# Performance work log

Hardware: AMD Instinct MI355X
Metric: run time of the kernel (lower is better)

## Reference

```python
import jax, jax.numpy as jnp
import numpy as np

D_MODEL = 768
MIMO_RANK = 4


def setup_inputs() -> dict:
    key = jax.random.key(0)
    ks = jax.random.split(key, 6)
    B, T, D, R = 2, 2048, D_MODEL, MIMO_RANK
    x = jax.random.normal(ks[0], (B, T, D), dtype=jnp.float32)
    norm_w = jnp.ones((D,), dtype=jnp.float32)
    W_in = jax.random.normal(ks[1], (D * R * 2, D), dtype=jnp.float32) * 0.02
    W_out = jax.random.normal(ks[2], (D, D), dtype=jnp.float32) * 0.02
    a_param = jax.random.normal(ks[3], (D, R, 2), dtype=jnp.float32) * 0.12
    b_param = jax.random.normal(ks[4], (D, R, 2), dtype=jnp.float32) * 0.15
    c_param = jax.random.normal(ks[5], (D, R, 2), dtype=jnp.float32) * 0.15
    return {"x": x, "norm_w": norm_w, "W_in": W_in, "W_out": W_out,
            "a_param": a_param, "b_param": b_param, "c_param": c_param}


def reference(x, norm_w, W_in, W_out, a_param, b_param, c_param):
    B, T, D = x.shape
    R = a_param.shape[1]
    # RMSNorm
    xn = x * jax.lax.rsqrt(jnp.mean(x * x, axis=-1, keepdims=True) + 1e-6) * norm_w
    # in_proj -> interleaved complex MIMO input u: [B,T,D,R,2]
    u = (xn @ W_in.T).reshape(B, T, D, R, 2)
    # coefficients (tanh-bounded; |a| scaled by 0.97 for stability)
    a = jnp.tanh(a_param) * 0.97
    b = jnp.tanh(b_param)
    c = jnp.tanh(c_param)
    ac = jax.lax.complex(a[..., 0], a[..., 1])  # [D,R]
    bc = jax.lax.complex(b[..., 0], b[..., 1])
    cc = jax.lax.complex(c[..., 0], c[..., 1])
    uc = jax.lax.complex(u[..., 0], u[..., 1])  # [B,T,D,R]
    # linear complex recurrence s_t = a * s_{t-1} + b * u_t, zero init state,
    # parallelized with an associative scan over time.
    bu = bc[None, None] * uc
    A = jnp.broadcast_to(ac[None, None], bu.shape)

    def comb(l, r):
        return (l[0] * r[0], r[0] * l[1] + r[1])

    _, s = jax.lax.associative_scan(comb, (A, bu), axis=1)  # [B,T,D,R] complex
    # output mix: real part of c * h, summed over MIMO rank -> [B,T,D]
    y = jnp.real(cc[None, None] * s).sum(axis=-1)
    return y @ W_out.T
```

## Files before the change

kernel.cpp:

```cpp
#include <hip/hip_runtime.h>
#include <hip/hip_bf16.h>
#include <stdint.h>

#define BATCH 2
#define TT 2048
#define DM 768
#define RR 4
#define M_TOK 4096
#define NFEAT 6144
#define NCH 6144
#define CHUNK 64
#define NCHUNK 32

typedef __attribute__((ext_vector_type(8))) short short8;
typedef __attribute__((ext_vector_type(4))) float float4v;

__device__ inline float bf2f(uint32_t bits16) {
    union { uint32_t u; float f; } x; x.u = bits16 << 16; return x.f;
}

typedef const __attribute__((address_space(1))) void* gptr_t;
typedef __attribute__((address_space(3))) void* lptr_t;

__device__ inline void async_ld16(const void* g, void* l) {
    __builtin_amdgcn_global_load_lds((gptr_t)(uintptr_t)g, (lptr_t)(uintptr_t)l,
                                     16, 0, 0);
}

__device__ inline void store_c(__hip_bfloat16* C, size_t idx, float v) {
    C[idx] = __float2bfloat16(v);
}
__device__ inline void store_c(float* C, size_t idx, float v) { C[idx] = v; }

__device__ inline uint2 pack4bf(float a, float b, float c, float d) {
    union { __hip_bfloat16 h[4]; uint2 u; } o;
    o.h[0] = __float2bfloat16(a); o.h[1] = __float2bfloat16(b);
    o.h[2] = __float2bfloat16(c); o.h[3] = __float2bfloat16(d);
    return o.u;
}

__device__ inline float2 cmul(float2 a, float2 b) {
    return make_float2(a.x * b.x - a.y * b.y, a.x * b.y + a.y * b.x);
}
__device__ inline float2 cmad(float2 a, float2 b, float2 c) {
    return make_float2(a.x * b.x - a.y * b.y + c.x,
                       a.x * b.y + a.y * b.x + c.y);
}
__device__ inline float2 csq(float2 a) {
    return make_float2(a.x * a.x - a.y * a.y, 2.f * a.x * a.y);
}

__device__ inline void cstep(float& sr, float& si, float2 a, float2 bb,
                             uint32_t uw) {
    float ur = bf2f(uw & 0xffffu), ui = bf2f(uw >> 16);
    float tr = bb.x * ur - bb.y * ui;
    float ti = bb.x * ui + bb.y * ur;
    float nr = a.x * sr - a.y * si + tr;
    float ni = a.x * si + a.y * sr + ti;
    sr = nr; si = ni;
}

__global__ __launch_bounds__(256) void prep_rms(
    const float* __restrict__ x, const float* __restrict__ w,
    const float* __restrict__ W_in, const float* __restrict__ W_out,
    const float* __restrict__ ap, const float* __restrict__ bp,
    const float* __restrict__ cp,
    __hip_bfloat16* __restrict__ xn,
    __hip_bfloat16* __restrict__ Win_bf, __hip_bfloat16* __restrict__ Wout_bf,
    float2* __restrict__ ac, float2* __restrict__ bc,
    float2* __restrict__ cc, float2* __restrict__ aL) {
    int bid = blockIdx.x;
    int tid = threadIdx.x;
    if (bid < M_TOK) {
        __shared__ float wsum[3];
        float4 v = make_float4(0.f, 0.f, 0.f, 0.f);
        if (tid < 192) v = ((const float4*)(x + (size_t)bid * DM))[tid];
        float ss = v.x * v.x + v.y * v.y + v.z * v.z + v.w * v.w;
        #pragma unroll
        for (int o = 1; o < 64; o <<= 1) ss += __shfl_xor(ss, o);
        if (tid < 192 && (tid & 63) == 0) wsum[tid >> 6] = ss;
        __syncthreads();
        if (tid < 192) {
            float tot = wsum[0] + wsum[1] + wsum[2];
            float scale = rsqrtf(tot * (1.f / DM) + 1e-6f);
            float4 wv = ((const float4*)w)[tid];
            ((uint2*)(xn + (size_t)bid * DM))[tid] =
                pack4bf(v.x * scale * wv.x, v.y * scale * wv.y,
                        v.z * scale * wv.z, v.w * scale * wv.w);
        }
        return;
    }
    const int N1 = NFEAT * DM / 4;
    const int N2 = DM * DM / 4;
    int i = (bid - M_TOK) * 256 + tid;
    if (i < N1) {
        float4 v = ((const float4*)W_in)[i];
        ((uint2*)Win_bf)[i] = pack4bf(v.x, v.y, v.z, v.w);
    } else if (i < N1 + N2) {
        int k = i - N1;
        float4 v = ((const float4*)W_out)[k];
        ((uint2*)Wout_bf)[k] = pack4bf(v.x, v.y, v.z, v.w);
    }
    if (i < DM * RR) {
        float ar = tanhf(ap[2 * i])     * 0.97f;
        float ai = tanhf(ap[2 * i + 1]) * 0.97f;
        ac[i] = make_float2(ar, ai);
        bc[i] = make_float2(tanhf(bp[2 * i]), tanhf(bp[2 * i + 1]));
        cc[i] = make_float2(tanhf(cp[2 * i]), tanhf(cp[2 * i + 1]));
        float xr = ar, xi = ai;
        #pragma unroll
        for (int k = 0; k < 6; ++k) {
            float nr = xr * xr - xi * xi;
            float ni = 2.f * xr * xi;
            xr = nr; xi = ni;
        }
        aL[i] = make_float2(xr, xi);
    }
}

template <int BM, int BN, int BK, typename OutT>
__device__ inline void gemm_body(
    const __hip_bfloat16* __restrict__ A, const __hip_bfloat16* __restrict__ B,
    OutT* __restrict__ C, int K, int ldc) {
    constexpr int MI = BM / 32;
    constexpr int NJ = BN / 32;
    constexpr int CPR = BK / 8;
    __shared__ __attribute__((aligned(16))) __hip_bfloat16 lA[BM * BK];
    __shared__ __attribute__((aligned(16))) __hip_bfloat16 lB[BN * BK];
    const int tid  = threadIdx.x;
    const int lane = tid & 63;
    const int wave = tid >> 6;
    const int quad = lane >> 4;
    const int l15  = lane & 15;
    const int wm = (wave >> 1) * (BM / 2);
    const int wn = (wave & 1) * (BN / 2);
    const int m0 = blockIdx.y * BM;
    const int n0 = blockIdx.x * BN;

    float4v acc[MI][NJ] = {};

    for (int k0 = 0; k0 < K; k0 += BK) {
        __syncthreads();
        #pragma unroll
        for (int it = 0; it < BM * CPR / 256; ++it) {
            int p = it * 256 + tid;
            int row = p / CPR;
            int cg = (p & (CPR - 1)) ^ (row & (CPR - 1));
            async_ld16(A + (size_t)(m0 + row) * K + k0 + cg * 8, lA + p * 8);
        }
        #pragma unroll
        for (int it = 0; it < BN * CPR / 256; ++it) {
            int p = it * 256 + tid;
            int row = p / CPR;
            int cg = (p & (CPR - 1)) ^ (row & (CPR - 1));
            async_ld16(B + (size_t)(n0 + row) * K + k0 + cg * 8, lB + p * 8);
        }
        __syncthreads();
        #pragma unroll
        for (int s = 0; s < BK / 32; ++s) {
            short8 af[MI], bfr[NJ];
            #pragma unroll
            for (int i = 0; i < MI; ++i) {
                int r = wm + i * 16 + l15;
                int c = (s * 4 + quad) ^ (r & (CPR - 1));
                af[i] = *(const short8*)(lA + r * BK + c * 8);
            }
            #pragma unroll
            for (int j = 0; j < NJ; ++j) {
                int r = wn + j * 16 + l15;
                int c = (s * 4 + quad) ^ (r & (CPR - 1));
                bfr[j] = *(const short8*)(lB + r * BK + c * 8);
            }
            #pragma unroll
            for (int i = 0; i < MI; ++i)
                #pragma unroll
                for (int j = 0; j < NJ; ++j)
                    acc[i][j] = __builtin_amdgcn_mfma_f32_16x16x32_bf16(
                        af[i], bfr[j], acc[i][j], 0, 0, 0);
        }
    }
    #pragma unroll
    for (int i = 0; i < MI; ++i)
        #pragma unroll
        for (int j = 0; j < NJ; ++j)
            #pragma unroll
            for (int rg = 0; rg < 4; ++rg) {
                int row = m0 + wm + i * 16 + quad * 4 + rg;
                int col = n0 + wn + j * 16 + l15;
                store_c(C, (size_t)row * ldc + col, acc[i][j][rg]);
            }
}

__global__ __launch_bounds__(256) void gemm_in(
    const __hip_bfloat16* __restrict__ A, const __hip_bfloat16* __restrict__ B,
    __hip_bfloat16* __restrict__ C, int K) {
    gemm_body<128, 128, 64, __hip_bfloat16>(A, B, C, K, NFEAT);
}

__global__ __launch_bounds__(256) void gemm_out(
    const __hip_bfloat16* __restrict__ A, const __hip_bfloat16* __restrict__ B,
    float* __restrict__ C, int K) {
    gemm_body<64, 64, 128, float>(A, B, C, K, DM);
}

__global__ __launch_bounds__(256) void scan_local2(
    const uint4* __restrict__ u4,
    const float2* __restrict__ ac, const float2* __restrict__ bc,
    const float2* __restrict__ cc,
    __hip_bfloat16* __restrict__ y_local,
    float2* __restrict__ chunkEnd) {
    __shared__ float2 se[1024];
    const int tid   = threadIdx.x;
    const int d_loc = tid & 31;
    const int s8    = tid >> 5;
    const int bd    = blockIdx.x;
    const int b     = bd >= 24;
    const int dg    = bd - b * 24;
    const int d_g   = dg * 32 + d_loc;
    const int cb    = d_g * RR;
    const int j     = blockIdx.y;

    float2 a0 = ac[cb], a1 = ac[cb + 1], a2 = ac[cb + 2], a3 = ac[cb + 3];
    float2 b0 = bc[cb], b1 = bc[cb + 1], b2 = bc[cb + 2], b3 = bc[cb + 3];
    float2 c0 = cc[cb], c1 = cc[cb + 1], c2 = cc[cb + 2], c3 = cc[cb + 3];

    const int token0 = b * TT + j * CHUNK + s8 * 8;
    const size_t base = (size_t)token0 * DM + d_g;

    uint4 uw[8];
    #pragma unroll
    for (int i = 0; i < 8; ++i) uw[i] = u4[base + (size_t)i * DM];
    float s0r = 0, s0i = 0, s1r = 0, s1i = 0;
    float s2r = 0, s2i = 0, s3r = 0, s3i = 0;
    float yloc[8];
    #pragma unroll
    for (int i = 0; i < 8; ++i) {
        cstep(s0r, s0i, a0, b0, uw[i].x);
        cstep(s1r, s1i, a1, b1, uw[i].y);
        cstep(s2r, s2i, a2, b2, uw[i].z);
        cstep(s3r, s3i, a3, b3, uw[i].w);
        yloc[i] = c0.x * s0r - c0.y * s0i + c1.x * s1r - c1.y * s1i
                + c2.x * s2r - c2.y * s2i + c3.x * s3r - c3.y * s3i;
    }
    se[tid * 4]     = make_float2(s0r, s0i);
    se[tid * 4 + 1] = make_float2(s1r, s1i);
    se[tid * 4 + 2] = make_float2(s2r, s2i);
    se[tid * 4 + 3] = make_float2(s3r, s3i);
    __syncthreads();

    float2 aE0 = csq(csq(csq(a0))), aE1 = csq(csq(csq(a1)));
    float2 aE2 = csq(csq(csq(a2))), aE3 = csq(csq(csq(a3)));
    float2 C0 = make_float2(0, 0), C1 = C0, C2 = C0, C3 = C0;
    for (int k = 0; k < s8; ++k) {
        int kb = (k * 32 + d_loc) * 4;
        C0 = cmad(C0, aE0, se[kb]);
        C1 = cmad(C1, aE1, se[kb + 1]);
        C2 = cmad(C2, aE2, se[kb + 2]);
        C3 = cmad(C3, aE3, se[kb + 3]);
    }
    if (s8 == 7) {
        size_t eb = (size_t)j * NCH + b * (DM * RR) + cb;
        chunkEnd[eb]     = cmad(C0, aE0, make_float2(s0r, s0i));
        chunkEnd[eb + 1] = cmad(C1, aE1, make_float2(s1r, s1i));
        chunkEnd[eb + 2] = cmad(C2, aE2, make_float2(s2r, s2i));
        chunkEnd[eb + 3] = cmad(C3, aE3, make_float2(s3r, s3i));
    }
    float2 q0 = cmul(cmul(c0, C0), a0);
    float2 q1 = cmul(cmul(c1, C1), a1);
    float2 q2 = cmul(cmul(c2, C2), a2);
    float2 q3 = cmul(cmul(c3, C3), a3);
    #pragma unroll
    for (int i = 0; i < 8; ++i) {
        float yv = yloc[i] + q0.x + q1.x + q2.x + q3.x;
        y_local[base + (size_t)i * DM] = __float2bfloat16(yv);
        q0 = cmul(q0, a0); q1 = cmul(q1, a1);
        q2 = cmul(q2, a2); q3 = cmul(q3, a3);
    }
}

__global__ __launch_bounds__(256) void carry_scan(
    float2* __restrict__ chunkEnd,
    const float2* __restrict__ aLp) {
    int ch = blockIdx.x * 256 + threadIdx.x;
    int dr = (ch >= DM * RR) ? ch - DM * RR : ch;
    float2 aL = aLp[dr];
    float2 K = make_float2(0.f, 0.f);
    for (int j = 0; j < NCHUNK; ++j) {
        size_t idx = (size_t)j * NCH + ch;
        float2 e = chunkEnd[idx];
        chunkEnd[idx] = K;
        K = cmad(K, aL, e);
    }
}

__global__ __launch_bounds__(256) void scan_fix(
    __hip_bfloat16* __restrict__ y_local,
    const float2* __restrict__ ac, const float2* __restrict__ cc,
    const float2* __restrict__ carry) {
    const int tid   = threadIdx.x;
    const int d_loc = tid & 31;
    const int s8    = tid >> 5;
    const int bd    = blockIdx.x;
    const int b     = bd >= 24;
    const int dg    = bd - b * 24;
    const int d_g   = dg * 32 + d_loc;
    const int cb    = d_g * RR;
    const int j     = blockIdx.y;
    const size_t kb = (size_t)j * NCH + b * (DM * RR) + cb;

    float2 a0 = ac[cb], a1 = ac[cb + 1], a2 = ac[cb + 2], a3 = ac[cb + 3];
    float2 c0 = cc[cb], c1 = cc[cb + 1], c2 = cc[cb + 2], c3 = cc[cb + 3];
    float2 K0 = carry[kb],     K1 = carry[kb + 1];
    float2 K2 = carry[kb + 2], K3 = carry[kb + 3];

    float2 aE0 = csq(csq(csq(a0))), aE1 = csq(csq(csq(a1)));
    float2 aE2 = csq(csq(csq(a2))), aE3 = csq(csq(csq(a3)));
    float2 q0 = cmul(cmul(c0, K0), a0);
    float2 q1 = cmul(cmul(c1, K1), a1);
    float2 q2 = cmul(cmul(c2, K2), a2);
    float2 q3 = cmul(cmul(c3, K3), a3);
    for (int t = 0; t < s8; ++t) {
        q0 = cmul(q0, aE0); q1 = cmul(q1, aE1);
        q2 = cmul(q2, aE2); q3 = cmul(q3, aE3);
    }
    const int token0 = b * TT + j * CHUNK + s8 * 8;
    const size_t base = (size_t)token0 * DM + d_g;
    #pragma unroll
    for (int i = 0; i < 8; ++i) {
        size_t idx = base + (size_t)i * DM;
        float yv = bf2f(((const uint16_t*)y_local)[idx])
                 + q0.x + q1.x + q2.x + q3.x;
        y_local[idx] = __float2bfloat16(yv);
        q0 = cmul(q0, a0); q1 = cmul(q1, a1);
        q2 = cmul(q2, a2); q3 = cmul(q3, a3);
    }
}

extern "C" void kernel_launch(void* const* d_in, const int* in_sizes, int n_in,
                              void* d_out, int out_size, void* d_ws,
                              size_t ws_size, hipStream_t stream) {
    const float* x      = (const float*)d_in[0];
    const float* norm_w = (const float*)d_in[1];
    const float* W_in   = (const float*)d_in[2];
    const float* W_out  = (const float*)d_in[3];
    const float* a_p    = (const float*)d_in[4];
    const float* b_p    = (const float*)d_in[5];
    const float* c_p    = (const float*)d_in[6];
    float* out = (float*)d_out;

    char* ws = (char*)d_ws;
    size_t off = 0;
    auto alloc = [&](size_t bytes) {
        void* p = ws + off;
        off += (bytes + 255) & ~(size_t)255;
        return p;
    };
    __hip_bfloat16* Win_bf  = (__hip_bfloat16*)alloc((size_t)NFEAT * DM * 2);
    __hip_bfloat16* Wout_bf = (__hip_bfloat16*)alloc((size_t)DM * DM * 2);
    __hip_bfloat16* xn      = (__hip_bfloat16*)alloc((size_t)M_TOK * DM * 2);
    __hip_bfloat16* u       = (__hip_bfloat16*)alloc((size_t)M_TOK * NFEAT * 2);
    __hip_bfloat16* y_local = (__hip_bfloat16*)alloc((size_t)M_TOK * DM * 2);
    float2* ac = (float2*)alloc((size_t)DM * RR * 8);
    float2* bc = (float2*)alloc((size_t)DM * RR * 8);
    float2* cc = (float2*)alloc((size_t)DM * RR * 8);
    float2* aL = (float2*)alloc((size_t)DM * RR * 8);
    float2* chunkEnd = (float2*)alloc((size_t)NCHUNK * NCH * 8);

    {
        int cast_blocks = ((NFEAT * DM + DM * DM) / 4 + 255) / 256;
        prep_rms<<<M_TOK + cast_blocks, 256, 0, stream>>>(
            x, norm_w, W_in, W_out, a_p, b_p, c_p,
            xn, Win_bf, Wout_bf, ac, bc, cc, aL);
    }
    gemm_in<<<dim3(NFEAT / 128, M_TOK / 128), 256, 0, stream>>>(
        xn, Win_bf, u, DM);
    scan_local2<<<dim3(48, NCHUNK), 256, 0, stream>>>(
        (const uint4*)u, ac, bc, cc, y_local, chunkEnd);
    carry_scan<<<NCH / 256, 256, 0, stream>>>(chunkEnd, aL);
    scan_fix<<<dim3(48, NCHUNK), 256, 0, stream>>>(
        y_local, ac, cc, chunkEnd);
    gemm_out<<<dim3(DM / 64, M_TOK / 64), 256, 0, stream>>>(
        y_local, Wout_bf, out, DM);
}
```

Before: 172.1 us.

## Double-buffer LDS tiles in input-projection GEMM with async loads

Replaces the generic gemm_body call in gemm_in with an inlined kernel that keeps two LDS buffers. It issues async global-to-LDS loads for the next K tile while MFMAs run on the current one, and uses a partial vmcnt wait. The goal is to hide global memory latency behind compute in the largest GEMM. In exchange the kernel uses twice the LDS, which may lower occupancy, and depends on hand-placed waitcnt and barrier ordering being correct.

```diff
diff --git a/kernel.cpp b/kernel.cpp
--- a/kernel.cpp
+++ b/kernel.cpp
@@ -194,7 +194,91 @@
 __global__ __launch_bounds__(256) void gemm_in(
     const __hip_bfloat16* __restrict__ A, const __hip_bfloat16* __restrict__ B,
     __hip_bfloat16* __restrict__ C, int K) {
-    gemm_body<128, 128, 64, __hip_bfloat16>(A, B, C, K, NFEAT);
+    constexpr int BM = 128, BN = 128, BK = 64;
+    constexpr int MI = BM / 32, NJ = BN / 32, CPR = BK / 8;
+    constexpr int ldc = NFEAT;
+    __shared__ __attribute__((aligned(16))) __hip_bfloat16
+        lds2[2][BM * BK + BN * BK];
+    const int tid  = threadIdx.x;
+    const int lane = tid & 63;
+    const int wave = tid >> 6;
+    const int quad = lane >> 4;
+    const int l15  = lane & 15;
+    const int wm = (wave >> 1) * (BM / 2);
+    const int wn = (wave & 1) * (BN / 2);
+    const int m0 = blockIdx.y * BM;
+    const int n0 = blockIdx.x * BN;
+
+    float4v acc[MI][NJ] = {};
+
+    auto stage = [&](int bi, int t) {
+        __hip_bfloat16* sA = lds2[bi];
+        __hip_bfloat16* sB = lds2[bi] + BM * BK;
+        const int k0 = t * BK;
+        #pragma unroll
+        for (int it = 0; it < BM * CPR / 256; ++it) {
+            int p = it * 256 + tid;
+            int row = p / CPR;
+            int cg = (p & (CPR - 1)) ^ (row & (CPR - 1));
+            async_ld16(A + (size_t)(m0 + row) * K + k0 + cg * 8, sA + p * 8);
+        }
+        #pragma unroll
+        for (int it = 0; it < BN * CPR / 256; ++it) {
+            int p = it * 256 + tid;
+            int row = p / CPR;
+            int cg = (p & (CPR - 1)) ^ (row & (CPR - 1));
+            async_ld16(B + (size_t)(n0 + row) * K + k0 + cg * 8, sB + p * 8);
+        }
+    };
+
+    const int nt = K / BK;
+    stage(0, 0);
+    for (int t = 0; t < nt; ++t) {
+        const int cur = t & 1;
+        if (t + 1 < nt) {
+            stage(cur ^ 1, t + 1);
+            asm volatile("s_waitcnt vmcnt(8)" ::: "memory");
+        } else {
+            asm volatile("s_waitcnt vmcnt(0)" ::: "memory");
+        }
+        asm volatile("s_barrier" ::: "memory");
+        const __hip_bfloat16* lA = lds2[cur];
+        const __hip_bfloat16* lB = lds2[cur] + BM * BK;
+        #pragma unroll
+        for (int s = 0; s < BK / 32; ++s) {
+            short8 af[MI], bfr[NJ];
+            #pragma unroll
+            for (int i = 0; i < MI; ++i) {
+                int r = wm + i * 16 + l15;
+                int c = (s * 4 + quad) ^ (r & (CPR - 1));
+                af[i] = *(const short8*)(lA + r * BK + c * 8);
+            }
+            #pragma unroll
+            for (int j = 0; j < NJ; ++j) {
+                int r = wn + j * 16 + l15;
+                int c = (s * 4 + quad) ^ (r & (CPR - 1));
+                bfr[j] = *(const short8*)(lB + r * BK + c * 8);
+            }
+            #pragma unroll
+            for (int i = 0; i < MI; ++i)
+                #pragma unroll
+                for (int j = 0; j < NJ; ++j)
+                    acc[i][j] = __builtin_amdgcn_mfma_f32_16x16x32_bf16(
+                        af[i], bfr[j], acc[i][j], 0, 0, 0);
+        }
+        asm volatile("s_waitcnt lgkmcnt(0)" ::: "memory");
+        asm volatile("s_barrier" ::: "memory");
+    }
+    #pragma unroll
+    for (int i = 0; i < MI; ++i)
+        #pragma unroll
+        for (int j = 0; j < NJ; ++j)
+            #pragma unroll
+            for (int rg = 0; rg < 4; ++rg) {
+                int row = m0 + wm + i * 16 + quad * 4 + rg;
+                int col = n0 + wn + j * 16 + l15;
+                store_c(C, (size_t)row * ldc + col, acc[i][j][rg]);
+            }
 }
 
 __global__ __launch_bounds__(256) void gemm_out(
```

New measurement: 171.1 us. No clear change (-0.6%).
